# Kernel optimization log

Hardware: AMD Instinct MI355X
Metric: run time of the kernel (lower is better)

Reference implementation:

```python
import jax, jax.numpy as jnp
import numpy as np

D = 128        # node_representation_size
V = 100000     # unique_internal_nodes (embedding vocab)
N = 20000      # nodes in the internal graph
E = 640000     # total neighbor (edge) entries


def setup_inputs() -> dict:
    key = jax.random.key(0)
    k1, k2, k3, k4, k5, k6 = jax.random.split(key, 6)
    node_ids = jax.random.randint(k1, (N,), 0, V)
    neighbor_ids = jax.random.randint(k2, (E,), 0, V)
    segment_ids = jnp.sort(jax.random.randint(k3, (E,), 0, N))
    xav = 1.0 / np.sqrt(D)  # xavier_normal std for square [D,D]
    W = jax.random.normal(k4, (D, D), dtype=jnp.float32) * xav
    M = jax.random.normal(k5, (D, D), dtype=jnp.float32) * xav
    emb = jax.random.normal(k6, (V, D), dtype=jnp.float32)
    return {"node_ids": node_ids, "neighbor_ids": neighbor_ids,
            "segment_ids": segment_ids, "W": W, "M": M, "emb": emb}


def reference(node_ids, neighbor_ids, segment_ids, W, M, emb):
    # Per node: s = relu(W @ e[node] + sum_{nbr} M @ e[nbr]); result = sum_nodes s
    self_term = emb[node_ids] @ W.T                       # [N, D]
    nb_msgs = emb[neighbor_ids] @ M.T                     # [E, D]
    nb_agg = jax.ops.segment_sum(nb_msgs, segment_ids, num_segments=N)  # [N, D]
    per_node = jax.nn.relu(self_term + nb_agg)            # [N, D]
    result = per_node.sum(axis=0)                         # [D]
    return jax.nn.softmax(result)[:, None]                # [D, 1], softmax over dim 0
```

## Files before the change

kernel.cpp:

```cpp
#include <hip/hip_runtime.h>

#define D 128
#define RS_STRIDE 64

typedef __attribute__((ext_vector_type(8))) short bf16x8;
typedef __attribute__((ext_vector_type(8))) unsigned short u16x8;
typedef __attribute__((ext_vector_type(4))) float f32x4;

__device__ __forceinline__ unsigned short f2bf(float f) {
    unsigned u = __float_as_uint(f);
    unsigned r = (u + 0x7fffu + ((u >> 16) & 1u)) >> 16;
    return (unsigned short)r;
}
__device__ __forceinline__ float bf2f(unsigned short h) {
    return __uint_as_float(((unsigned)h) << 16);
}
__device__ __forceinline__ ushort4 pack4(float4 v) {
    ushort4 o; o.x = f2bf(v.x); o.y = f2bf(v.y); o.z = f2bf(v.z); o.w = f2bf(v.w);
    return o;
}
__device__ __forceinline__ void red3(float& x) {
    x += __shfl_xor(x, 8);
    x += __shfl_xor(x, 16);
    x += __shfl_xor(x, 32);
}

__global__ void convert_kernel(const float* __restrict__ emb, const float* __restrict__ W,
                               const float* __restrict__ M, unsigned short* __restrict__ embb,
                               unsigned short* __restrict__ Wb, unsigned short* __restrict__ Mb,
                               float* __restrict__ rs, int n4) {
    int i = blockIdx.x * blockDim.x + threadIdx.x;
    if (i < n4) ((ushort4*)embb)[i] = pack4(((const float4*)emb)[i]);
    if (i < 4096)       ((ushort4*)Wb)[i]        = pack4(((const float4*)W)[i]);
    else if (i < 8192)  ((ushort4*)Mb)[i - 4096] = pack4(((const float4*)M)[i - 4096]);
    if (i < D) rs[i * RS_STRIDE] = 0.0f;
}

__global__ void rowptr_kernel(const int* __restrict__ seg, int* __restrict__ row_ptr,
                              int E, int N) {
    int e = blockIdx.x * blockDim.x + threadIdx.x;
    if (e >= E) return;
    int s = seg[e];
    if (e == 0) {
        for (int n = 0; n <= s; ++n) row_ptr[n] = 0;
    } else {
        int sp = seg[e - 1];
        for (int n = sp + 1; n <= s; ++n) row_ptr[n] = e;
    }
    if (e == E - 1) {
        for (int n = s + 1; n <= N; ++n) row_ptr[n] = E;
    }
}

__global__ void agg_bf_kernel(const int* __restrict__ nbr, const int* __restrict__ row_ptr,
                              const unsigned short* __restrict__ embb,
                              unsigned short* __restrict__ aggb, int N) {
    int n = blockIdx.x * 4 + (threadIdx.x >> 6);
    if (n >= N) return;
    int tt = threadIdx.x & 63;
    int c = tt & 7;
    int j = tt >> 3;

    int lo = row_ptr[n], hi = row_ptr[n + 1];

    float s0[8], s1[8];
#pragma unroll
    for (int k = 0; k < 8; ++k) { s0[k] = 0.f; s1[k] = 0.f; }

    for (int e = lo + j; e < hi; e += 8) {
        const u16x8* r = (const u16x8*)(embb + (size_t)nbr[e] * D);
        u16x8 v0 = r[c];
        u16x8 v1 = r[c + 8];
#pragma unroll
        for (int k = 0; k < 8; ++k) { s0[k] += bf2f(v0[k]); s1[k] += bf2f(v1[k]); }
    }
#pragma unroll
    for (int k = 0; k < 8; ++k) { red3(s0[k]); red3(s1[k]); }

    if (j == 0) {
        u16x8 o0, o1;
#pragma unroll
        for (int k = 0; k < 8; ++k) { o0[k] = f2bf(s0[k]); o1[k] = f2bf(s1[k]); }
        u16x8* o = (u16x8*)(aggb + (size_t)n * D);
        o[c] = o0;
        o[c + 8] = o1;
    }
}

__global__ void agg_f32_kernel(const int* __restrict__ nbr, const int* __restrict__ row_ptr,
                               const float* __restrict__ emb,
                               unsigned short* __restrict__ aggb, int N) {
    int n = blockIdx.x * 4 + (threadIdx.x >> 6);
    if (n >= N) return;
    int tt = threadIdx.x & 63;
    int c = tt & 7;
    int j = tt >> 3;

    int lo = row_ptr[n], hi = row_ptr[n + 1];

    float4 s0 = make_float4(0.f, 0.f, 0.f, 0.f);
    float4 s1 = make_float4(0.f, 0.f, 0.f, 0.f);
    float4 s2 = make_float4(0.f, 0.f, 0.f, 0.f);
    float4 s3 = make_float4(0.f, 0.f, 0.f, 0.f);
    for (int e = lo + j; e < hi; e += 8) {
        const float4* r = (const float4*)&emb[(size_t)nbr[e] * D];
        float4 v0 = r[c], v1 = r[c + 8], v2 = r[c + 16], v3 = r[c + 24];
        s0.x += v0.x; s0.y += v0.y; s0.z += v0.z; s0.w += v0.w;
        s1.x += v1.x; s1.y += v1.y; s1.z += v1.z; s1.w += v1.w;
        s2.x += v2.x; s2.y += v2.y; s2.z += v2.z; s2.w += v2.w;
        s3.x += v3.x; s3.y += v3.y; s3.z += v3.z; s3.w += v3.w;
    }
    red3(s0.x); red3(s0.y); red3(s0.z); red3(s0.w);
    red3(s1.x); red3(s1.y); red3(s1.z); red3(s1.w);
    red3(s2.x); red3(s2.y); red3(s2.z); red3(s2.w);
    red3(s3.x); red3(s3.y); red3(s3.z); red3(s3.w);
    if (j == 0) {
        ushort4* o = (ushort4*)(aggb + (size_t)n * D);
        o[c]      = pack4(s0);
        o[c + 8]  = pack4(s1);
        o[c + 16] = pack4(s2);
        o[c + 24] = pack4(s3);
    }
}

template <bool BF>
__global__ __launch_bounds__(256) void matvec_kernel(
    const int* __restrict__ node_ids, const void* __restrict__ embv,
    const unsigned short* __restrict__ aggb,
    const unsigned short* __restrict__ Wb, const unsigned short* __restrict__ Mb,
    float* __restrict__ rs, int N, int ngroups, int nstripes) {
    int t = threadIdx.x;
    int wid = blockIdx.x * 4 + (t >> 6);
    int l = t & 63;
    int quad = l >> 4, col = l & 15;
    int dt = wid & 7;
    int stripe = wid >> 3;

    bf16x8 bw[4], bm[4];
    int wrow = (dt * 16 + col) * D;
#pragma unroll
    for (int ks = 0; ks < 4; ++ks) {
        int off = wrow + ks * 32 + quad * 8;
        bw[ks] = *(const bf16x8*)(Wb + off);
        bm[ks] = *(const bf16x8*)(Mb + off);
    }

    const bf16x8 zero8 = {0, 0, 0, 0, 0, 0, 0, 0};
    float vsum = 0.f;

    for (int grp = stripe; grp < ngroups; grp += nstripes) {
        int node = grp * 16 + col;
        bool valid = node < N;
        int nid = valid ? node_ids[node] : 0;
        const unsigned short* ar = aggb + (size_t)node * D + quad * 8;

        f32x4 acc = {0.f, 0.f, 0.f, 0.f};
#pragma unroll
        for (int ks = 0; ks < 4; ++ks) {
            bf16x8 ax;
            if (BF) {
                const unsigned short* xr =
                    (const unsigned short*)embv + (size_t)nid * D + quad * 8;
                ax = valid ? *(const bf16x8*)(xr + ks * 32) : zero8;
            } else {
                if (valid) {
                    const float4* xf = (const float4*)((const float*)embv +
                                       (size_t)nid * D + quad * 8 + ks * 32);
                    ushort4 p0 = pack4(xf[0]);
                    ushort4 p1 = pack4(xf[1]);
                    ax[0] = (short)p0.x; ax[1] = (short)p0.y;
                    ax[2] = (short)p0.z; ax[3] = (short)p0.w;
                    ax[4] = (short)p1.x; ax[5] = (short)p1.y;
                    ax[6] = (short)p1.z; ax[7] = (short)p1.w;
                } else ax = zero8;
            }
            bf16x8 aa = valid ? *(const bf16x8*)(ar + ks * 32) : zero8;
            acc = __builtin_amdgcn_mfma_f32_16x16x32_bf16(ax, bw[ks], acc, 0, 0, 0);
            acc = __builtin_amdgcn_mfma_f32_16x16x32_bf16(aa, bm[ks], acc, 0, 0, 0);
        }
        vsum += fmaxf(acc[0], 0.f) + fmaxf(acc[1], 0.f)
              + fmaxf(acc[2], 0.f) + fmaxf(acc[3], 0.f);
    }

    vsum += __shfl_xor(vsum, 16);
    vsum += __shfl_xor(vsum, 32);
    if (l < 16) atomicAdd(&rs[(dt * 16 + col) * RS_STRIDE], vsum);
}

__global__ void softmax_kernel(const float* __restrict__ rs, float* __restrict__ out) {
    int t = threadIdx.x;
    float v0 = rs[t * RS_STRIDE];
    float v1 = rs[(t + 64) * RS_STRIDE];
    float m = fmaxf(v0, v1);
    for (int o = 32; o > 0; o >>= 1) m = fmaxf(m, __shfl_xor(m, o));
    float e0 = expf(v0 - m);
    float e1 = expf(v1 - m);
    float s = e0 + e1;
    for (int o = 32; o > 0; o >>= 1) s += __shfl_xor(s, o);
    float inv = 1.0f / s;
    out[t] = e0 * inv;
    out[t + 64] = e1 * inv;
}

extern "C" void kernel_launch(void* const* d_in, const int* in_sizes, int n_in,
                              void* d_out, int out_size, void* d_ws, size_t ws_size,
                              hipStream_t stream) {
    const int*   node_ids = (const int*)d_in[0];
    const int*   nbr      = (const int*)d_in[1];
    const int*   seg      = (const int*)d_in[2];
    const float* W        = (const float*)d_in[3];
    const float* M        = (const float*)d_in[4];
    const float* emb      = (const float*)d_in[5];
    float* out = (float*)d_out;

    int N = in_sizes[0];
    int E = in_sizes[1];
    long long VD = in_sizes[5];
    int ngroups  = (N + 15) / 16;
    int nstripes = (ngroups + 1) / 2;
    int mv_blocks = 2 * nstripes;

    unsigned short* aggb = (unsigned short*)d_ws;
    unsigned short* Wb   = aggb + (size_t)N * D;
    unsigned short* Mb   = Wb + D * D;
    float* rs            = (float*)(Mb + D * D);
    int* row_ptr         = (int*)(rs + (size_t)D * RS_STRIDE);
    unsigned short* embb = (unsigned short*)(row_ptr + (N + 1));

    size_t need_bf = (size_t)(row_ptr + (N + 1) - (int*)d_ws) * 4 + (size_t)VD * 2;
    bool use_bf = ws_size >= need_bf;
    int n4 = use_bf ? (int)(VD / 4) : 0;
    int cvt_n = (n4 > 8192 ? n4 : 8192);

    convert_kernel<<<(cvt_n + 255) / 256, 256, 0, stream>>>(emb, W, M, embb, Wb, Mb, rs, n4);
    rowptr_kernel<<<(E + 255) / 256, 256, 0, stream>>>(seg, row_ptr, E, N);
    if (use_bf) {
        agg_bf_kernel<<<(N + 3) / 4, 256, 0, stream>>>(nbr, row_ptr, embb, aggb, N);
        matvec_kernel<true><<<mv_blocks, 256, 0, stream>>>(node_ids, embb, aggb, Wb, Mb,
                                                           rs, N, ngroups, nstripes);
    } else {
        agg_f32_kernel<<<(N + 3) / 4, 256, 0, stream>>>(nbr, row_ptr, emb, aggb, N);
        matvec_kernel<false><<<mv_blocks, 256, 0, stream>>>(node_ids, emb, aggb, Wb, Mb,
                                                            rs, N, ngroups, nstripes);
    }
    softmax_kernel<<<1, 64, 0, stream>>>(rs, out);
}
```

Before: 153.1 us.

## Fuse convert and rowptr kernels; widen bf16 gather with 16 edges per wave and prefetch

Merges the bf16 conversion kernel and the CSR row-pointer kernel into a single prep launch, removing one launch and its dependency gap. The bf16 aggregation kernel now has each lane cover 32 of the 128 columns, so 16 edges are in flight per wave instead of 8, and the next neighbor index is fetched before the current row is accumulated to hide index-load latency. This adds register pressure (32 float accumulators) and one extra shuffle stage in the reduction. The f32 fallback's reduction is only restructured.

```diff
diff --git a/kernel.cpp b/kernel.cpp
--- a/kernel.cpp
+++ b/kernel.cpp
@@ -19,36 +19,28 @@
     ushort4 o; o.x = f2bf(v.x); o.y = f2bf(v.y); o.z = f2bf(v.z); o.w = f2bf(v.w);
     return o;
 }
-__device__ __forceinline__ void red3(float& x) {
-    x += __shfl_xor(x, 8);
-    x += __shfl_xor(x, 16);
-    x += __shfl_xor(x, 32);
-}
-
-__global__ void convert_kernel(const float* __restrict__ emb, const float* __restrict__ W,
-                               const float* __restrict__ M, unsigned short* __restrict__ embb,
-                               unsigned short* __restrict__ Wb, unsigned short* __restrict__ Mb,
-                               float* __restrict__ rs, int n4) {
+
+__global__ void prep_kernel(const float* __restrict__ emb, const float* __restrict__ W,
+                            const float* __restrict__ M, const int* __restrict__ seg,
+                            unsigned short* __restrict__ embb, unsigned short* __restrict__ Wb,
+                            unsigned short* __restrict__ Mb, float* __restrict__ rs,
+                            int* __restrict__ row_ptr, int n4, int E, int N) {
     int i = blockIdx.x * blockDim.x + threadIdx.x;
     if (i < n4) ((ushort4*)embb)[i] = pack4(((const float4*)emb)[i]);
     if (i < 4096)       ((ushort4*)Wb)[i]        = pack4(((const float4*)W)[i]);
     else if (i < 8192)  ((ushort4*)Mb)[i - 4096] = pack4(((const float4*)M)[i - 4096]);
     if (i < D) rs[i * RS_STRIDE] = 0.0f;
-}
-
-__global__ void rowptr_kernel(const int* __restrict__ seg, int* __restrict__ row_ptr,
-                              int E, int N) {
-    int e = blockIdx.x * blockDim.x + threadIdx.x;
-    if (e >= E) return;
-    int s = seg[e];
-    if (e == 0) {
-        for (int n = 0; n <= s; ++n) row_ptr[n] = 0;
-    } else {
-        int sp = seg[e - 1];
-        for (int n = sp + 1; n <= s; ++n) row_ptr[n] = e;
-    }
-    if (e == E - 1) {
-        for (int n = s + 1; n <= N; ++n) row_ptr[n] = E;
+    if (i < E) {
+        int s = seg[i];
+        if (i == 0) {
+            for (int n = 0; n <= s; ++n) row_ptr[n] = 0;
+        } else {
+            int sp = seg[i - 1];
+            for (int n = sp + 1; n <= s; ++n) row_ptr[n] = i;
+        }
+        if (i == E - 1) {
+            for (int n = s + 1; n <= N; ++n) row_ptr[n] = E;
+        }
     }
 }
 
@@ -58,32 +50,54 @@
     int n = blockIdx.x * 4 + (threadIdx.x >> 6);
     if (n >= N) return;
     int tt = threadIdx.x & 63;
-    int c = tt & 7;
-    int j = tt >> 3;
+    int c = tt & 3;
+    int j = tt >> 2;
 
     int lo = row_ptr[n], hi = row_ptr[n + 1];
 
-    float s0[8], s1[8];
-#pragma unroll
-    for (int k = 0; k < 8; ++k) { s0[k] = 0.f; s1[k] = 0.f; }
-
-    for (int e = lo + j; e < hi; e += 8) {
-        const u16x8* r = (const u16x8*)(embb + (size_t)nbr[e] * D);
-        u16x8 v0 = r[c];
-        u16x8 v1 = r[c + 8];
-#pragma unroll
-        for (int k = 0; k < 8; ++k) { s0[k] += bf2f(v0[k]); s1[k] += bf2f(v1[k]); }
-    }
-#pragma unroll
-    for (int k = 0; k < 8; ++k) { red3(s0[k]); red3(s1[k]); }
+    float s[4][8];
+#pragma unroll
+    for (int q = 0; q < 4; ++q)
+#pragma unroll
+        for (int k = 0; k < 8; ++k) s[q][k] = 0.f;
+
+    int e = lo + j;
+    int id = (e < hi) ? nbr[e] : -1;
+    while (id >= 0) {
+        const u16x8* r = (const u16x8*)(embb + (size_t)id * D);
+        int e2 = e + 16;
+        int id2 = (e2 < hi) ? nbr[e2] : -1;
+        u16x8 v0 = r[c], v1 = r[c + 4], v2 = r[c + 8], v3 = r[c + 12];
+#pragma unroll
+        for (int k = 0; k < 8; ++k) {
+            s[0][k] += bf2f((unsigned short)v0[k]);
+            s[1][k] += bf2f((unsigned short)v1[k]);
+            s[2][k] += bf2f((unsigned short)v2[k]);
+            s[3][k] += bf2f((unsigned short)v3[k]);
+        }
+        e = e2; id = id2;
+    }
+#pragma unroll
+    for (int q = 0; q < 4; ++q)
+#pragma unroll
+        for (int k = 0; k < 8; ++k) {
+            float x = s[q][k];
+            x += __shfl_xor(x, 4);
+            x += __shfl_xor(x, 8);
+            x += __shfl_xor(x, 16);
+            x += __shfl_xor(x, 32);
+            s[q][k] = x;
+        }
 
     if (j == 0) {
-        u16x8 o0, o1;
-#pragma unroll
-        for (int k = 0; k < 8; ++k) { o0[k] = f2bf(s0[k]); o1[k] = f2bf(s1[k]); }
         u16x8* o = (u16x8*)(aggb + (size_t)n * D);
-        o[c] = o0;
-        o[c + 8] = o1;
+#pragma unroll
+        for (int q = 0; q < 4; ++q) {
+            u16x8 ov;
+#pragma unroll
+            for (int k = 0; k < 8; ++k) ov[k] = f2bf(s[q][k]);
+            o[c + 4 * q] = ov;
+        }
     }
 }
 
@@ -110,10 +124,17 @@
         s2.x += v2.x; s2.y += v2.y; s2.z += v2.z; s2.w += v2.w;
         s3.x += v3.x; s3.y += v3.y; s3.z += v3.z; s3.w += v3.w;
     }
-    red3(s0.x); red3(s0.y); red3(s0.z); red3(s0.w);
-    red3(s1.x); red3(s1.y); red3(s1.z); red3(s1.w);
-    red3(s2.x); red3(s2.y); red3(s2.z); red3(s2.w);
-    red3(s3.x); red3(s3.y); red3(s3.z); red3(s3.w);
+#pragma unroll
+    for (int o = 8; o <= 32; o <<= 1) {
+        s0.x += __shfl_xor(s0.x, o); s0.y += __shfl_xor(s0.y, o);
+        s0.z += __shfl_xor(s0.z, o); s0.w += __shfl_xor(s0.w, o);
+        s1.x += __shfl_xor(s1.x, o); s1.y += __shfl_xor(s1.y, o);
+        s1.z += __shfl_xor(s1.z, o); s1.w += __shfl_xor(s1.w, o);
+        s2.x += __shfl_xor(s2.x, o); s2.y += __shfl_xor(s2.y, o);
+        s2.z += __shfl_xor(s2.z, o); s2.w += __shfl_xor(s2.w, o);
+        s3.x += __shfl_xor(s3.x, o); s3.y += __shfl_xor(s3.y, o);
+        s3.z += __shfl_xor(s3.z, o); s3.w += __shfl_xor(s3.w, o);
+    }
     if (j == 0) {
         ushort4* o = (ushort4*)(aggb + (size_t)n * D);
         o[c]      = pack4(s0);
@@ -230,10 +251,12 @@
     size_t need_bf = (size_t)(row_ptr + (N + 1) - (int*)d_ws) * 4 + (size_t)VD * 2;
     bool use_bf = ws_size >= need_bf;
     int n4 = use_bf ? (int)(VD / 4) : 0;
-    int cvt_n = (n4 > 8192 ? n4 : 8192);
-
-    convert_kernel<<<(cvt_n + 255) / 256, 256, 0, stream>>>(emb, W, M, embb, Wb, Mb, rs, n4);
-    rowptr_kernel<<<(E + 255) / 256, 256, 0, stream>>>(seg, row_ptr, E, N);
+    int prep_n = n4;
+    if (prep_n < E) prep_n = E;
+    if (prep_n < 8192) prep_n = 8192;
+
+    prep_kernel<<<(prep_n + 255) / 256, 256, 0, stream>>>(emb, W, M, seg, embb, Wb, Mb,
+                                                          rs, row_ptr, n4, E, N);
     if (use_bf) {
         agg_bf_kernel<<<(N + 3) / 4, 256, 0, stream>>>(nbr, row_ptr, embb, aggb, N);
         matvec_kernel<true><<<mv_blocks, 256, 0, stream>>>(node_ids, embb, aggb, Wb, Mb,
```

Result: no change. 155.3 us (+1.4%).
